# Optimization experiments

Hardware: AMD Instinct MI355X
Metric: run time of the kernel (lower is better)

The kernel has to match this reference:

```python
import jax, jax.numpy as jnp
import numpy as np


def setup_inputs() -> dict:
    key = jax.random.key(0)
    ks = jax.random.split(key, 6)
    T, F, INPUT_SIZE = 32768, 758, 730  # F = input_size + attributes(27) + 1(catch_ID)
    return {
        "x": jax.random.normal(ks[0], (T, F), dtype=jnp.float32),
        "weight_input": jax.random.normal(ks[1], (4, INPUT_SIZE), dtype=jnp.float32) * 0.05,
        "weight_recur": jax.random.normal(ks[2], (4, 1), dtype=jnp.float32) * 0.05,
        "bias": jax.random.normal(ks[3], (4, 1), dtype=jnp.float32) * 0.05,
        "reg_w": jax.random.normal(ks[4], (1, 1), dtype=jnp.float32),
        "reg_b": jax.random.normal(ks[5], (1,), dtype=jnp.float32),
        "h0": jnp.zeros((1,), dtype=jnp.float32),
        "c0": jnp.zeros((1,), dtype=jnp.float32),
    }


def reference(x, weight_input, weight_recur, bias, reg_w, reg_b, h0, c0):
    input_size = weight_input.shape[1]
    # x[:, :-attributes-1] in the original == first input_size columns
    x_feat = x[:, :input_size]                      # [T, input_size]
    # hoist the per-step mm(weight_input, x_t) into one GEMM: [T, 4]
    xp = x_feat @ weight_input.T
    wr = weight_recur[:, 0]                         # [4]
    b = bias[:, 0]                                  # [4]

    def step(carry, xp_t):
        h, c = carry                                # scalars (state_size == 1)
        gates = b + wr * h + xp_t                   # [4]
        f = jax.nn.sigmoid(gates[0])
        i = jax.nn.sigmoid(gates[1])
        o = jax.nn.sigmoid(gates[2])
        g = jnp.tanh(gates[3])
        c1 = f * c + i * g
        h1 = o * jnp.tanh(c1)
        return (h1, c1), (h1, c1)

    (_, _), (hs, cs) = jax.lax.scan(step, (h0[0], c0[0]), xp)
    h_n = jnp.concatenate([h0[None, :], hs[:, None]], axis=0)  # [T+1, 1]
    c_n = jnp.concatenate([c0[None, :], cs[:, None]], axis=0)  # [T+1, 1]
    q_t = (h_n @ reg_w.T + reg_b)[1:]                          # [T, 1]
    return q_t, h_n, c_n
```

## Files before the change

kernel.cpp:

```cpp
#include <hip/hip_runtime.h>

#define T_LEN 32768
#define F_DIM 758
#define IN_SZ 730
#define CHUNK_L 16
#define WARM_W 64
#define N_CHUNK (T_LEN / CHUNK_L)
#define SCAN_BLOCKS (N_CHUNK / 64)
#define STAGE_ROWS 1088

#define GEMV_BLOCKS 512
#define GEMV_WAVES (GEMV_BLOCKS * 4)
#define ROWS_PER_WAVE (T_LEN / GEMV_WAVES)

__global__ __launch_bounds__(256) void gemv_gates(
    const float* __restrict__ x, const float* __restrict__ w,
    const float* __restrict__ bias, float* __restrict__ xpw) {
  const float L2E = 1.4426950408889634f;
  int lane = threadIdx.x & 63;
  int g    = lane & 3;
  int p    = lane >> 2;
  int wid  = (blockIdx.x * 256 + threadIdx.x) >> 6;

  const float* wg = w + (size_t)g * IN_SZ;
  float4 wv[12];
#pragma unroll
  for (int j = 0; j < 12; j++) {
    int c = p + 16 * j;
#pragma unroll
    for (int e = 0; e < 4; e++) {
      int k = 4 * c + e;
      ((float*)&wv[j])[e] = (k < IN_SZ) ? wg[k] : 0.f;
    }
  }
  float bg = bias[g];
  float cg = (g == 3) ? (-2.f * L2E) : (-L2E);

  const float4 z4 = {0.f, 0.f, 0.f, 0.f};
  float4 xa[12], xb[12];

  auto loadrow = [&](float4* dst, int row) {
    const float* xr = x + (size_t)row * F_DIM;
#pragma unroll
    for (int j = 0; j < 12; j++) {
      int c = p + 16 * j;
      dst[j] = (c < 183) ? *(const float4*)(xr + 4 * c) : z4;
    }
  };
  auto dot = [&](const float4* v) {
    float s = 0.f;
#pragma unroll
    for (int j = 0; j < 12; j++) {
      s = fmaf(v[j].x, wv[j].x, s);
      s = fmaf(v[j].y, wv[j].y, s);
      s = fmaf(v[j].z, wv[j].z, s);
      s = fmaf(v[j].w, wv[j].w, s);
    }
    s += __shfl_xor(s, 4);
    s += __shfl_xor(s, 8);
    s += __shfl_xor(s, 16);
    s += __shfl_xor(s, 32);
    return s;
  };

  loadrow(xa, wid);
  loadrow(xb, wid + GEMV_WAVES);
#pragma unroll
  for (int r = 0; r < ROWS_PER_WAVE; r += 2) {
    float sA = dot(xa);
    if (r + 2 < ROWS_PER_WAVE) loadrow(xa, wid + GEMV_WAVES * (r + 2));
    if (lane < 4) xpw[(size_t)(wid + GEMV_WAVES * r) * 4 + lane] = cg * (sA + bg);
    float sB = dot(xb);
    if (r + 3 < ROWS_PER_WAVE) loadrow(xb, wid + GEMV_WAVES * (r + 3));
    if (lane < 4) xpw[(size_t)(wid + GEMV_WAVES * (r + 1)) * 4 + lane] = cg * (sB + bg);
  }
}

__device__ __forceinline__ int phys(int r) {
  return (r & ~15) | ((r + (r >> 4)) & 15);
}

__global__ __launch_bounds__(64) void lstm_scan(
    const float* __restrict__ xpw, const float* __restrict__ wr,
    const float* __restrict__ rgw, const float* __restrict__ rgb,
    const float* __restrict__ h0p, const float* __restrict__ c0p,
    float* __restrict__ out) {
  const float L2E = 1.4426950408889634f;
  const float M2  = -2.f * L2E;
  __shared__ float4 lds_xp[STAGE_ROWS];
  __shared__ float  lds_h[64][17];
  __shared__ float  lds_c[64][17];

  int lane = threadIdx.x;
  int B0   = blockIdx.x * (64 * CHUNK_L);
  int R0   = B0 - WARM_W; if (R0 < 0) R0 = 0;

  const float4* xp4 = (const float4*)xpw;
#pragma unroll
  for (int i = 0; i < STAGE_ROWS / 64; i++) {
    int r = 64 * i + lane;
    lds_xp[phys(r)] = xp4[R0 + r];
  }
  __syncthreads();

  float w20 = -L2E * wr[0];
  float w21 = -L2E * wr[1];
  float w22 = -L2E * wr[2];
  float w23 = -2.f * L2E * wr[3];

  float h = h0p[0], c = c0p[0];

  auto stepc = [&](float4 p) {
    float u0 = fmaf(h, w20, p.x);
    float u1 = fmaf(h, w21, p.y);
    float u2 = fmaf(h, w22, p.z);
    float u3 = fmaf(h, w23, p.w);
    float f  = __builtin_amdgcn_rcpf(1.f + __builtin_amdgcn_exp2f(u0));
    float i  = __builtin_amdgcn_rcpf(1.f + __builtin_amdgcn_exp2f(u1));
    float o  = __builtin_amdgcn_rcpf(1.f + __builtin_amdgcn_exp2f(u2));
    float r3 = __builtin_amdgcn_rcpf(1.f + __builtin_amdgcn_exp2f(u3));
    c = fmaf(f, c, fmaf(2.f * i, r3, -i));
    float rt = __builtin_amdgcn_rcpf(1.f + __builtin_amdgcn_exp2f(c * M2));
    h = fmaf(2.f * o, rt, -o);
  };

  auto XP = [&](int r) {
    int rc = r < 0 ? 0 : (r > STAGE_ROWS - 1 ? STAGE_ROWS - 1 : r);
    return lds_xp[phys(rc)];
  };

  int start = B0 + lane * CHUNK_L;
  int rr = (start - WARM_W) - R0;

  float4 p0 = XP(rr), p1 = XP(rr + 1), p2 = XP(rr + 2), p3 = XP(rr + 3);

  for (int s = 0; s < WARM_W; s += 4, rr += 4) {
    float4 n0 = XP(rr + 4), n1 = XP(rr + 5), n2 = XP(rr + 6), n3 = XP(rr + 7);
    if (rr     >= 0) stepc(p0);
    if (rr + 1 >= 0) stepc(p1);
    if (rr + 2 >= 0) stepc(p2);
    if (rr + 3 >= 0) stepc(p3);
    p0 = n0; p1 = n1; p2 = n2; p3 = n3;
  }
#pragma unroll
  for (int gq = 0; gq < CHUNK_L; gq += 4, rr += 4) {
    float4 n0 = XP(rr + 4), n1 = XP(rr + 5), n2 = XP(rr + 6), n3 = XP(rr + 7);
    stepc(p0); lds_h[lane][gq + 0] = h; lds_c[lane][gq + 0] = c;
    stepc(p1); lds_h[lane][gq + 1] = h; lds_c[lane][gq + 1] = c;
    stepc(p2); lds_h[lane][gq + 2] = h; lds_c[lane][gq + 2] = c;
    stepc(p3); lds_h[lane][gq + 3] = h; lds_c[lane][gq + 3] = c;
    p0 = n0; p1 = n1; p2 = n2; p3 = n3;
  }
  __syncthreads();

  float* outq = out;
  float* outh = out + T_LEN;
  float* outc = out + 2 * T_LEN + 1;
  float rw = rgw[0], rb = rgb[0];
#pragma unroll
  for (int k = 0; k < CHUNK_L; k++) {
    int idx = lane + 64 * k;
    float hv = lds_h[idx >> 4][idx & 15];
    float cv = lds_c[idx >> 4][idx & 15];
    outq[B0 + idx]     = fmaf(hv, rw, rb);
    outh[B0 + idx + 1] = hv;
    outc[B0 + idx + 1] = cv;
  }
  if (blockIdx.x == 0 && lane == 0) { outh[0] = h0p[0]; outc[0] = c0p[0]; }
}

extern "C" void kernel_launch(void* const* d_in, const int* in_sizes, int n_in,
                              void* d_out, int out_size, void* d_ws, size_t ws_size,
                              hipStream_t stream) {
  const float* x  = (const float*)d_in[0];
  const float* wi = (const float*)d_in[1];
  const float* wr = (const float*)d_in[2];
  const float* bs = (const float*)d_in[3];
  const float* rw = (const float*)d_in[4];
  const float* rb = (const float*)d_in[5];
  const float* h0 = (const float*)d_in[6];
  const float* c0 = (const float*)d_in[7];
  float* out = (float*)d_out;
  float* xpw = (float*)d_ws;

  gemv_gates<<<GEMV_BLOCKS, 256, 0, stream>>>(x, wi, bs, xpw);
  lstm_scan<<<SCAN_BLOCKS, 64, 0, stream>>>(xpw, wr, rw, rb, h0, c0, out);
}
```

Before: 32.98 us.

## Restructure gate GEMV to process row pairs with one gate per wave

Rewrites the input-projection GEMV so that each wave owns one gate and all four waves of a block read the same pair of consecutive rows. The pair is loaded as one contiguous span of 379 float4, which gives aligned vector loads across the row boundary and lets the four waves share loads through cache. Weights are pre-split per lane into two masked copies, one per row. The change adds a full 64-lane shuffle reduction and quadruple redundant x reads per block, paying extra FMAs on zeroed weights in exchange for fully coalesced contiguous loads.

```diff
diff --git a/kernel.cpp b/kernel.cpp
--- a/kernel.cpp
+++ b/kernel.cpp
@@ -9,70 +9,84 @@
 #define SCAN_BLOCKS (N_CHUNK / 64)
 #define STAGE_ROWS 1088
 
-#define GEMV_BLOCKS 512
-#define GEMV_WAVES (GEMV_BLOCKS * 4)
-#define ROWS_PER_WAVE (T_LEN / GEMV_WAVES)
+#define PAIRS (T_LEN / 2)
+#define GEMV_BLOCKS 1024
+#define PAIRS_PER_BLOCK (PAIRS / GEMV_BLOCKS)
 
 __global__ __launch_bounds__(256) void gemv_gates(
     const float* __restrict__ x, const float* __restrict__ w,
     const float* __restrict__ bias, float* __restrict__ xpw) {
   const float L2E = 1.4426950408889634f;
-  int lane = threadIdx.x & 63;
-  int g    = lane & 3;
-  int p    = lane >> 2;
-  int wid  = (blockIdx.x * 256 + threadIdx.x) >> 6;
+  int tid  = threadIdx.x;
+  int lane = tid & 63;
+  int g    = tid >> 6;
 
   const float* wg = w + (size_t)g * IN_SZ;
-  float4 wv[12];
-#pragma unroll
-  for (int j = 0; j < 12; j++) {
-    int c = p + 16 * j;
+  float wA[6][4], wB[6][4];
+#pragma unroll
+  for (int s = 0; s < 6; s++) {
+    int q = lane + 64 * s;
 #pragma unroll
     for (int e = 0; e < 4; e++) {
-      int k = 4 * c + e;
-      ((float*)&wv[j])[e] = (k < IN_SZ) ? wg[k] : 0.f;
+      int idx = 4 * q + e;
+      int r01 = idx / 758;
+      int k   = idx - 758 * r01;
+      float val = (q < 379 && r01 < 2 && k < IN_SZ) ? wg[k] : 0.f;
+      wA[s][e] = (r01 == 0) ? val : 0.f;
+      wB[s][e] = (r01 == 1) ? val : 0.f;
     }
   }
   float bg = bias[g];
   float cg = (g == 3) ? (-2.f * L2E) : (-L2E);
 
   const float4 z4 = {0.f, 0.f, 0.f, 0.f};
-  float4 xa[12], xb[12];
-
-  auto loadrow = [&](float4* dst, int row) {
-    const float* xr = x + (size_t)row * F_DIM;
-#pragma unroll
-    for (int j = 0; j < 12; j++) {
-      int c = p + 16 * j;
-      dst[j] = (c < 183) ? *(const float4*)(xr + 4 * c) : z4;
-    }
-  };
-  auto dot = [&](const float4* v) {
-    float s = 0.f;
-#pragma unroll
-    for (int j = 0; j < 12; j++) {
-      s = fmaf(v[j].x, wv[j].x, s);
-      s = fmaf(v[j].y, wv[j].y, s);
-      s = fmaf(v[j].z, wv[j].z, s);
-      s = fmaf(v[j].w, wv[j].w, s);
-    }
-    s += __shfl_xor(s, 4);
-    s += __shfl_xor(s, 8);
-    s += __shfl_xor(s, 16);
-    s += __shfl_xor(s, 32);
-    return s;
-  };
-
-  loadrow(xa, wid);
-  loadrow(xb, wid + GEMV_WAVES);
-#pragma unroll
-  for (int r = 0; r < ROWS_PER_WAVE; r += 2) {
-    float sA = dot(xa);
-    if (r + 2 < ROWS_PER_WAVE) loadrow(xa, wid + GEMV_WAVES * (r + 2));
-    if (lane < 4) xpw[(size_t)(wid + GEMV_WAVES * r) * 4 + lane] = cg * (sA + bg);
-    float sB = dot(xb);
-    if (r + 3 < ROWS_PER_WAVE) loadrow(xb, wid + GEMV_WAVES * (r + 3));
-    if (lane < 4) xpw[(size_t)(wid + GEMV_WAVES * (r + 1)) * 4 + lane] = cg * (sB + bg);
+  float4 xa[6], xb[6];
+
+  auto loadpair = [&](float4* dst, int pr) {
+    const float4* src = (const float4*)x + (size_t)pr * 379;
+#pragma unroll
+    for (int s = 0; s < 6; s++) {
+      int q = lane + 64 * s;
+      dst[s] = (q < 379) ? src[q] : z4;
+    }
+  };
+  auto dotpair = [&](const float4* v, float& rA, float& rB) {
+    float sA = 0.f, sB = 0.f;
+#pragma unroll
+    for (int s = 0; s < 6; s++) {
+#pragma unroll
+      for (int e = 0; e < 4; e++) {
+        float xv = ((const float*)&v[s])[e];
+        sA = fmaf(xv, wA[s][e], sA);
+        sB = fmaf(xv, wB[s][e], sB);
+      }
+    }
+#pragma unroll
+    for (int off = 1; off < 64; off <<= 1) {
+      sA += __shfl_xor(sA, off);
+      sB += __shfl_xor(sB, off);
+    }
+    rA = sA; rB = sB;
+  };
+  auto emit = [&](int pr, float sA, float sB) {
+    if (lane == 0) {
+      xpw[(size_t)(2 * pr) * 4 + g]     = cg * (sA + bg);
+      xpw[(size_t)(2 * pr + 1) * 4 + g] = cg * (sB + bg);
+    }
+  };
+
+  int p0 = blockIdx.x;
+  loadpair(xa, p0);
+  loadpair(xb, p0 + GEMV_BLOCKS);
+#pragma unroll
+  for (int r = 0; r < PAIRS_PER_BLOCK; r += 2) {
+    float sA, sB;
+    dotpair(xa, sA, sB);
+    if (r + 2 < PAIRS_PER_BLOCK) loadpair(xa, p0 + (r + 2) * GEMV_BLOCKS);
+    emit(p0 + r * GEMV_BLOCKS, sA, sB);
+    dotpair(xb, sA, sB);
+    if (r + 3 < PAIRS_PER_BLOCK) loadpair(xb, p0 + (r + 3) * GEMV_BLOCKS);
+    emit(p0 + (r + 1) * GEMV_BLOCKS, sA, sB);
   }
 }
 
```

After: 43.95 us. +33.3%, slower.

## Process row pairs as contiguous float4 spans with LDS-staged shifted weights

Applied to the files above, without the earlier changes.

The GEMV now treats each pair of consecutive rows as one contiguous 1516-float span (379 float4s), which is 16-byte aligned because 758*2 is divisible by 4. Each lane loads six float4s that cover both rows, so every read is fully coalesced and no padded per-row columns are fetched. Two zero-padded, shifted copies of the weights are staged in LDS so that one pass computes all four gates for both rows, followed by shuffle reductions. The cost is extra LDS reads, more shuffles, and a larger block size of 512 threads, in exchange for fewer and more efficient global loads.

```diff
diff --git a/kernel.cpp b/kernel.cpp
--- a/kernel.cpp
+++ b/kernel.cpp
@@ -9,70 +9,94 @@
 #define SCAN_BLOCKS (N_CHUNK / 64)
 #define STAGE_ROWS 1088
 
-#define GEMV_BLOCKS 512
-#define GEMV_WAVES (GEMV_BLOCKS * 4)
-#define ROWS_PER_WAVE (T_LEN / GEMV_WAVES)
-
-__global__ __launch_bounds__(256) void gemv_gates(
+#define PAIRS 16384
+#define GEMV_BLOCKS 1024
+#define WAVES_TOTAL (GEMV_BLOCKS * 8)
+
+__device__ __forceinline__ float dot4(float4 a, float4 b, float acc) {
+  acc = fmaf(a.x, b.x, acc);
+  acc = fmaf(a.y, b.y, acc);
+  acc = fmaf(a.z, b.z, acc);
+  return fmaf(a.w, b.w, acc);
+}
+
+__global__ __launch_bounds__(512) void gemv_gates(
     const float* __restrict__ x, const float* __restrict__ w,
     const float* __restrict__ bias, float* __restrict__ xpw) {
   const float L2E = 1.4426950408889634f;
-  int lane = threadIdx.x & 63;
-  int g    = lane & 3;
-  int p    = lane >> 2;
-  int wid  = (blockIdx.x * 256 + threadIdx.x) >> 6;
-
-  const float* wg = w + (size_t)g * IN_SZ;
-  float4 wv[12];
-#pragma unroll
-  for (int j = 0; j < 12; j++) {
-    int c = p + 16 * j;
+  __shared__ float4 wp0[4][192];
+  __shared__ float4 wp1[4][384];
+  int tid  = threadIdx.x;
+  int lane = tid & 63;
+
+  for (int q = tid; q < 768; q += 512) {
+    int g = q / 192, c = q - 192 * g;
+    float4 v;
 #pragma unroll
     for (int e = 0; e < 4; e++) {
       int k = 4 * c + e;
-      ((float*)&wv[j])[e] = (k < IN_SZ) ? wg[k] : 0.f;
-    }
-  }
-  float bg = bias[g];
-  float cg = (g == 3) ? (-2.f * L2E) : (-L2E);
-
-  const float4 z4 = {0.f, 0.f, 0.f, 0.f};
-  float4 xa[12], xb[12];
-
-  auto loadrow = [&](float4* dst, int row) {
-    const float* xr = x + (size_t)row * F_DIM;
-#pragma unroll
-    for (int j = 0; j < 12; j++) {
-      int c = p + 16 * j;
-      dst[j] = (c < 183) ? *(const float4*)(xr + 4 * c) : z4;
-    }
-  };
-  auto dot = [&](const float4* v) {
-    float s = 0.f;
-#pragma unroll
-    for (int j = 0; j < 12; j++) {
-      s = fmaf(v[j].x, wv[j].x, s);
-      s = fmaf(v[j].y, wv[j].y, s);
-      s = fmaf(v[j].z, wv[j].z, s);
-      s = fmaf(v[j].w, wv[j].w, s);
-    }
-    s += __shfl_xor(s, 4);
+      ((float*)&v)[e] = (k < IN_SZ) ? w[g * IN_SZ + k] : 0.f;
+    }
+    wp0[g][c] = v;
+  }
+  for (int q = tid; q < 1536; q += 512) {
+    int g = q / 384, c = q - 384 * g;
+    float4 v;
+#pragma unroll
+    for (int e = 0; e < 4; e++) {
+      int f = 4 * c + e;
+      ((float*)&v)[e] = (f >= F_DIM && f < F_DIM + IN_SZ) ? w[g * IN_SZ + (f - F_DIM)] : 0.f;
+    }
+    wp1[g][c] = v;
+  }
+  __syncthreads();
+
+  int wid = blockIdx.x * 8 + (tid >> 6);
+#pragma unroll
+  for (int it = 0; it < 2; it++) {
+    int pr = wid + it * WAVES_TOTAL;
+    const float4* src = (const float4*)x + (size_t)pr * 379;
+    float4 xv[6];
+#pragma unroll
+    for (int m = 0; m < 6; m++) {
+      int q = lane + 64 * m;
+      if (q > 378) q = 378;
+      xv[m] = src[q];
+    }
+    float a0[4] = {0.f, 0.f, 0.f, 0.f};
+    float a1[4] = {0.f, 0.f, 0.f, 0.f};
+#pragma unroll
+    for (int g = 0; g < 4; g++) {
+      const float4* p0 = wp0[g];
+      const float4* p1 = wp1[g];
+      a0[g] = dot4(xv[0], p0[lane],       a0[g]);
+      a0[g] = dot4(xv[1], p0[lane + 64],  a0[g]);
+      a0[g] = dot4(xv[2], p0[lane + 128], a0[g]);
+      a1[g] = dot4(xv[2], p1[lane + 128], a1[g]);
+      a1[g] = dot4(xv[3], p1[lane + 192], a1[g]);
+      a1[g] = dot4(xv[4], p1[lane + 256], a1[g]);
+      a1[g] = dot4(xv[5], p1[lane + 320], a1[g]);
+    }
+#pragma unroll
+    for (int off = 1; off <= 4; off <<= 1) {
+#pragma unroll
+      for (int g = 0; g < 4; g++) {
+        a0[g] += __shfl_xor(a0[g], off);
+        a1[g] += __shfl_xor(a1[g], off);
+      }
+    }
+    int g = lane & 3, r = (lane >> 2) & 1;
+    float s0 = (g == 0) ? a0[0] : (g == 1) ? a0[1] : (g == 2) ? a0[2] : a0[3];
+    float s1 = (g == 0) ? a1[0] : (g == 1) ? a1[1] : (g == 2) ? a1[2] : a1[3];
+    float s  = r ? s1 : s0;
     s += __shfl_xor(s, 8);
     s += __shfl_xor(s, 16);
     s += __shfl_xor(s, 32);
-    return s;
-  };
-
-  loadrow(xa, wid);
-  loadrow(xb, wid + GEMV_WAVES);
-#pragma unroll
-  for (int r = 0; r < ROWS_PER_WAVE; r += 2) {
-    float sA = dot(xa);
-    if (r + 2 < ROWS_PER_WAVE) loadrow(xa, wid + GEMV_WAVES * (r + 2));
-    if (lane < 4) xpw[(size_t)(wid + GEMV_WAVES * r) * 4 + lane] = cg * (sA + bg);
-    float sB = dot(xb);
-    if (r + 3 < ROWS_PER_WAVE) loadrow(xb, wid + GEMV_WAVES * (r + 3));
-    if (lane < 4) xpw[(size_t)(wid + GEMV_WAVES * (r + 1)) * 4 + lane] = cg * (sB + bg);
+    if (lane < 8) {
+      float bg = bias[g];
+      float cg = (g == 3) ? (-2.f * L2E) : (-L2E);
+      xpw[(size_t)(2 * pr + r) * 4 + g] = cg * (s + bg);
+    }
   }
 }
 
@@ -183,6 +207,6 @@
   float* out = (float*)d_out;
   float* xpw = (float*)d_ws;
 
-  gemv_gates<<<GEMV_BLOCKS, 256, 0, stream>>>(x, wi, bs, xpw);
+  gemv_gates<<<GEMV_BLOCKS, 512, 0, stream>>>(x, wi, bs, xpw);
   lstm_scan<<<SCAN_BLOCKS, 64, 0, stream>>>(xpw, wr, rw, rb, h0, c0, out);
 }
```

Measured after the change: 35.30 us. 1.07x slower.

## Stage contiguous x row pairs into LDS via async global_load_lds double buffering

Applied to the files above, without the earlier changes.

The gate GEMV no longer loads each row's float4 slices straight into registers. Each block now streams contiguous 8-row batches of x into a double-buffered LDS tile with asynchronous global_load_lds. Each wave then computes two rows from LDS, reading the odd, misaligned row as float2 pairs. The aim is fully coalesced, contiguous global traffic with the next batch's load overlapping compute. In exchange it also reads the unused tail columns, uses 48KB of LDS per block (limiting occupancy), and relies on the barrier to wait for the async loads.

```diff
diff --git a/kernel.cpp b/kernel.cpp
--- a/kernel.cpp
+++ b/kernel.cpp
@@ -10,17 +10,20 @@
 #define STAGE_ROWS 1088
 
 #define GEMV_BLOCKS 512
-#define GEMV_WAVES (GEMV_BLOCKS * 4)
-#define ROWS_PER_WAVE (T_LEN / GEMV_WAVES)
+#define BATCHES 8
+#define B_CHUNKS 1516
+#define X_CHUNKS 6209536
 
 __global__ __launch_bounds__(256) void gemv_gates(
     const float* __restrict__ x, const float* __restrict__ w,
     const float* __restrict__ bias, float* __restrict__ xpw) {
   const float L2E = 1.4426950408889634f;
-  int lane = threadIdx.x & 63;
+  __shared__ float4 xbuf[2][1536];
+  int tid  = threadIdx.x;
+  int lane = tid & 63;
   int g    = lane & 3;
   int p    = lane >> 2;
-  int wid  = (blockIdx.x * 256 + threadIdx.x) >> 6;
+  int wv_i = tid >> 6;
 
   const float* wg = w + (size_t)g * IN_SZ;
   float4 wv[12];
@@ -30,49 +33,69 @@
 #pragma unroll
     for (int e = 0; e < 4; e++) {
       int k = 4 * c + e;
-      ((float*)&wv[j])[e] = (k < IN_SZ) ? wg[k] : 0.f;
+      ((float*)&wv[j])[e] = (c < 183 && k < IN_SZ) ? wg[k] : 0.f;
     }
   }
   float bg = bias[g];
   float cg = (g == 3) ? (-2.f * L2E) : (-L2E);
 
-  const float4 z4 = {0.f, 0.f, 0.f, 0.f};
-  float4 xa[12], xb[12];
-
-  auto loadrow = [&](float4* dst, int row) {
-    const float* xr = x + (size_t)row * F_DIM;
+  const float4* xg = (const float4*)x;
+
+  auto stage = [&](int b, int buf) {
+    size_t base = ((size_t)blockIdx.x * BATCHES + b) * B_CHUNKS;
+#pragma unroll
+    for (int s = 0; s < 6; s++) {
+      int q = tid + 256 * s;
+      size_t gi = base + (size_t)q;
+      if (gi > X_CHUNKS - 1) gi = X_CHUNKS - 1;
+      __builtin_amdgcn_global_load_lds(
+          (const __attribute__((address_space(1))) unsigned int*)(xg + gi),
+          (__attribute__((address_space(3))) unsigned int*)(&xbuf[buf][q]),
+          16, 0, 0);
+    }
+  };
+
+  auto compute = [&](int b, int buf) {
+    int P = (blockIdx.x * BATCHES + b) * 4 + wv_i;
+    const float4* pb4 = &xbuf[buf][wv_i * 379];
+    const float2* pb2 = (const float2*)pb4;
+    float s0 = 0.f, s1 = 0.f;
 #pragma unroll
     for (int j = 0; j < 12; j++) {
       int c = p + 16 * j;
-      dst[j] = (c < 183) ? *(const float4*)(xr + 4 * c) : z4;
-    }
-  };
-  auto dot = [&](const float4* v) {
-    float s = 0.f;
-#pragma unroll
-    for (int j = 0; j < 12; j++) {
-      s = fmaf(v[j].x, wv[j].x, s);
-      s = fmaf(v[j].y, wv[j].y, s);
-      s = fmaf(v[j].z, wv[j].z, s);
-      s = fmaf(v[j].w, wv[j].w, s);
-    }
-    s += __shfl_xor(s, 4);
-    s += __shfl_xor(s, 8);
-    s += __shfl_xor(s, 16);
-    s += __shfl_xor(s, 32);
-    return s;
-  };
-
-  loadrow(xa, wid);
-  loadrow(xb, wid + GEMV_WAVES);
-#pragma unroll
-  for (int r = 0; r < ROWS_PER_WAVE; r += 2) {
-    float sA = dot(xa);
-    if (r + 2 < ROWS_PER_WAVE) loadrow(xa, wid + GEMV_WAVES * (r + 2));
-    if (lane < 4) xpw[(size_t)(wid + GEMV_WAVES * r) * 4 + lane] = cg * (sA + bg);
-    float sB = dot(xb);
-    if (r + 3 < ROWS_PER_WAVE) loadrow(xb, wid + GEMV_WAVES * (r + 3));
-    if (lane < 4) xpw[(size_t)(wid + GEMV_WAVES * (r + 1)) * 4 + lane] = cg * (sB + bg);
+      if (c < 183) {
+        float4 v = pb4[c];
+        s0 = fmaf(v.x, wv[j].x, s0);
+        s0 = fmaf(v.y, wv[j].y, s0);
+        s0 = fmaf(v.z, wv[j].z, s0);
+        s0 = fmaf(v.w, wv[j].w, s0);
+        float2 lo = pb2[379 + 2 * c];
+        float2 hi = pb2[379 + 2 * c + 1];
+        s1 = fmaf(lo.x, wv[j].x, s1);
+        s1 = fmaf(lo.y, wv[j].y, s1);
+        s1 = fmaf(hi.x, wv[j].z, s1);
+        s1 = fmaf(hi.y, wv[j].w, s1);
+      }
+    }
+#pragma unroll
+    for (int off = 4; off < 64; off <<= 1) {
+      s0 += __shfl_xor(s0, off);
+      s1 += __shfl_xor(s1, off);
+    }
+    if (lane < 4) {
+      xpw[(size_t)(2 * P) * 4 + g]     = cg * (s0 + bg);
+      xpw[(size_t)(2 * P + 1) * 4 + g] = cg * (s1 + bg);
+    }
+  };
+
+  stage(0, 0);
+  __syncthreads();
+#pragma unroll
+  for (int b = 0; b < BATCHES; b++) {
+    int buf = b & 1;
+    if (b + 1 < BATCHES) stage(b + 1, buf ^ 1);
+    compute(b, buf);
+    __syncthreads();
   }
 }
 
```

Result: slower. 34.01 us (+3.1%).
